# Optimization experiments

Measured on AMD Instinct MI355X. Metric: run time of the kernel, lower is better.

Reference implementation:

```python
import jax, jax.numpy as jnp
import numpy as np

GROUP_SIZE = 128
IN_FEATURES = 4096
OUT_FEATURES = 11008
BATCH = 16


def setup_inputs() -> dict:
    key = jax.random.key(0)
    k_x, k_q, k_s, k_z, k_b = jax.random.split(key, 5)
    num_groups = IN_FEATURES // GROUP_SIZE
    x = jax.random.normal(k_x, (BATCH, IN_FEATURES), dtype=jnp.float32)
    # packed int4 pairs stored as bytes in [0, 256)
    qweight = jax.random.randint(k_q, (OUT_FEATURES, IN_FEATURES // 2), 0, 256, dtype=jnp.int32)
    # positive scales of realistic magnitude, zeros in [0, 15]
    scales = jax.random.uniform(k_s, (OUT_FEATURES, num_groups), dtype=jnp.float32) * 0.01 + 1e-4
    zeros = jax.random.uniform(k_z, (OUT_FEATURES, num_groups), dtype=jnp.float32) * 15.0
    bias = jax.random.normal(k_b, (OUT_FEATURES,), dtype=jnp.float32)
    return {"x": x, "qweight": qweight, "scales": scales, "zeros": zeros, "bias": bias}


def _unpack_int4(packed, in_features):
    # packed: [O, I//2] ints in [0,256); low nibble is even column, high nibble odd
    low = packed & 15
    high = (packed >> 4) & 15
    return jnp.stack([low, high], axis=-1).reshape(packed.shape[0], in_features)  # [O, I]


def reference(x, qweight, scales, zeros, bias):
    q = _unpack_int4(qweight, IN_FEATURES).astype(jnp.float32)        # [O, I]
    s = jnp.repeat(scales, GROUP_SIZE, axis=1)                        # [O, I]
    z = jnp.repeat(zeros, GROUP_SIZE, axis=1)                         # [O, I]
    w = (q - z) * s                                                   # dequantized weight [O, I]
    return x @ w.T + bias                                             # [B, O]
```

## Files before the change

kernel.cpp:

```cpp
#include <hip/hip_runtime.h>
#include <hip/hip_fp16.h>

#define IN_F   4096
#define OUT_F  11008
#define BATCH  16
#define GROUPS 32
#define PPR    2048

typedef __attribute__((ext_vector_type(8))) _Float16 half8;
typedef __attribute__((ext_vector_type(2))) _Float16 h2;
typedef __attribute__((ext_vector_type(4))) float    float4_t;
typedef __attribute__((ext_vector_type(4))) int      int4_t;
typedef __attribute__((ext_vector_type(4))) unsigned uint4_t;

__device__ inline h2 cvt2(float a, float b) {
    return __builtin_bit_cast(h2, __builtin_amdgcn_cvt_pkrtz(a, b));
}

#define GLOAD_LDS(srcp, ldsp) \
    __builtin_amdgcn_global_load_lds( \
        (const __attribute__((address_space(1))) void*)(srcp), \
        (__attribute__((address_space(3))) void*)(ldsp), 16, 0, 0)

__global__ __launch_bounds__(256) void xcvt_perm(const float* __restrict__ x,
                                                 _Float16* __restrict__ xp) {
    const int T = blockIdx.x * 256 + threadIdx.x;
    const int step = T >> 6, lane = T & 63;
    const int b = lane & 15, k = step * 32 + (lane >> 4) * 8;
    const float4_t a0 = *(const float4_t*)(x + b * IN_F + k);
    const float4_t a1 = *(const float4_t*)(x + b * IN_F + k + 4);
    half8 h;
    h2 p0 = cvt2(a0.x, a0.y), p1 = cvt2(a0.z, a0.w);
    h2 p2 = cvt2(a1.x, a1.y), p3 = cvt2(a1.z, a1.w);
    h[0]=p0[0]; h[1]=p0[1]; h[2]=p1[0]; h[3]=p1[1];
    h[4]=p2[0]; h[5]=p2[1]; h[6]=p3[0]; h[7]=p3[1];
    *(half8*)(xp + step * 512 + lane * 8) = h;
}

__global__ __launch_bounds__(256) void gptq_gemm_w(
    const _Float16* __restrict__ xp, const int* __restrict__ qw,
    const float* __restrict__ scales, const float* __restrict__ zeros,
    float* __restrict__ ws_part)
{
    __shared__ int   lq[16 * 512];
    __shared__ float red[4][16][17];

    const int tid  = threadIdx.x;
    const int lane = tid & 63, wave = tid >> 6;
    const int otile = blockIdx.x >> 2, kq = blockIdx.x & 3;
    const int ln = lane & 15, lk = lane >> 4;
    const int o  = otile * 16 + ln;

    #pragma unroll
    for (int i = 0; i < 4; ++i) {
        const int row = wave * 4 + i;
        const int* src = qw + (otile * 16 + row) * PPR + kq * 512
                       + ((lane ^ (row & 7)) * 4);
        GLOAD_LDS(src, &lq[row * 512]);
    }

    const int c = wave;
    const int g = kq * 8 + c * 2;
    const float s0 = scales[o * GROUPS + g], s1 = scales[o * GROUPS + g + 1];
    const float z0 = zeros [o * GROUPS + g], z1 = zeros [o * GROUPS + g + 1];
    const h2 s2[2] = { cvt2(s0, s0), cvt2(s1, s1) };
    const h2 c2[2] = { cvt2(-z0 * s0, -z0 * s0), cvt2(-z1 * s1, -z1 * s1) };
    const h2 k1024 = { (_Float16)1024.0f, (_Float16)1024.0f };
    const int x3 = ln & 7;

    float4_t acc = {0.f, 0.f, 0.f, 0.f};

#define COMPUTE(C) { \
    _Pragma("unroll") \
    for (int t = 0; t < 8; ++t) { \
        const int4_t v = *(const int4_t*)((const char*)lq + ln * 2048 \
                        + (((C) * 32 + ((t * 4 + lk) ^ x3)) << 4)); \
        const half8 af = *(const half8*)(xp + (kq * 32 + (C) * 8 + t) * 512 \
                        + lane * 8); \
        const int gi = t >> 2; \
        uint4_t bw; \
        _Pragma("unroll") \
        for (int i = 0; i < 4; ++i) { \
            const unsigned pv = (unsigned)v[i]; \
            const unsigned u = (pv & 0xFu) | ((pv << 12) & 0xF0000u) \
                             | 0x64006400u;             \
            h2 q = __builtin_bit_cast(h2, u) - k1024;   \
            h2 w = q * s2[gi] + c2[gi];                 \
            bw[i] = __builtin_bit_cast(unsigned, w); \
        } \
        acc = __builtin_amdgcn_mfma_f32_16x16x32_f16( \
            af, __builtin_bit_cast(half8, bw), acc, 0, 0, 0); \
    } }

    __syncthreads();

    #pragma unroll
    for (int i = 0; i < 4; ++i) {
        const int row = wave * 4 + i;
        const int* src = qw + (otile * 16 + row) * PPR + kq * 512 + 256
                       + ((lane ^ (row & 7)) * 4);
        GLOAD_LDS(src, &lq[row * 512 + 256]);
    }

    if (wave < 2) COMPUTE(c)

    __syncthreads();

    if (wave >= 2) COMPUTE(c)

    #pragma unroll
    for (int r = 0; r < 4; ++r) red[wave][lk * 4 + r][ln] = acc[r];
    __syncthreads();

    const int row = tid >> 4, col = tid & 15;
    const float sum = red[0][row][col] + red[1][row][col]
                    + red[2][row][col] + red[3][row][col];
    ws_part[(kq * BATCH + row) * OUT_F + otile * 16 + col] = sum;
#undef COMPUTE
}

__global__ __launch_bounds__(256) void gptq_reduce(
    const float* __restrict__ ws_part, const float* __restrict__ bias,
    float* __restrict__ out)
{
    const int idx = blockIdx.x * 256 + threadIdx.x;
    if (idx >= BATCH * OUT_F) return;
    const int o = idx % OUT_F;
    out[idx] = bias[o]
             + ws_part[idx]
             + ws_part[1 * (BATCH * OUT_F) + idx]
             + ws_part[2 * (BATCH * OUT_F) + idx]
             + ws_part[3 * (BATCH * OUT_F) + idx];
}

__global__ __launch_bounds__(256) void gptq_gemm_fb(
    const float* __restrict__ x, const int* __restrict__ qw,
    const float* __restrict__ scales, const float* __restrict__ zeros,
    const float* __restrict__ bias, float* __restrict__ out)
{
    const int tid  = threadIdx.x;
    const int lane = tid & 63;
    const int wave = tid >> 6;
    const int otile = blockIdx.x;
    const int ln = lane & 15, lk = lane >> 4;
    const int o = otile * 16 + ln;
    const int kc0 = wave * 1024;

    const int* qbase = qw + o * PPR + (kc0 >> 1) + lk * 4;
    const float* srow = scales + o * GROUPS;
    const float* zrow = zeros  + o * GROUPS;

    float4_t acc = {0.f, 0.f, 0.f, 0.f};
    const h2 k1024 = { (_Float16)1024.0f, (_Float16)1024.0f };

    #pragma unroll
    for (int ch = 0; ch < 4; ++ch) {
        const int cc = kc0 + ch * 256;
        h2 s2[2], c2[2];
        #pragma unroll
        for (int gi = 0; gi < 2; ++gi) {
            const float s  = srow[(cc >> 7) + gi];
            const float c0 = -zrow[(cc >> 7) + gi] * s;
            s2[gi] = cvt2(s, s); c2[gi] = cvt2(c0, c0);
        }
        #pragma unroll
        for (int t = 0; t < 8; ++t) {
            const int4_t v = *(const int4_t*)(qbase + ch * 128 + t * 16);
            const float* xq = x + ln * IN_F + cc + t * 32 + lk * 8;
            const float4_t a0 = *(const float4_t*)(xq);
            const float4_t a1 = *(const float4_t*)(xq + 4);
            half8 af;
            h2 p0 = cvt2(a0.x, a0.y), p1 = cvt2(a0.z, a0.w);
            h2 p2 = cvt2(a1.x, a1.y), p3 = cvt2(a1.z, a1.w);
            af[0]=p0[0]; af[1]=p0[1]; af[2]=p1[0]; af[3]=p1[1];
            af[4]=p2[0]; af[5]=p2[1]; af[6]=p3[0]; af[7]=p3[1];
            const int gi = t >> 2;
            uint4_t bw;
            #pragma unroll
            for (int i = 0; i < 4; ++i) {
                const unsigned pv = (unsigned)v[i];
                const unsigned u = (pv & 0xFu) | ((pv << 12) & 0xF0000u)
                                 | 0x64006400u;
                h2 q = __builtin_bit_cast(h2, u) - k1024;
                h2 w = q * s2[gi] + c2[gi];
                bw[i] = __builtin_bit_cast(unsigned, w);
            }
            acc = __builtin_amdgcn_mfma_f32_16x16x32_f16(
                af, __builtin_bit_cast(half8, bw), acc, 0, 0, 0);
        }
    }

    __shared__ float red[4][16][17];
    #pragma unroll
    for (int r = 0; r < 4; ++r) red[wave][lk * 4 + r][ln] = acc[r];
    __syncthreads();
    const int row = tid >> 4, col = tid & 15;
    const float sum = red[0][row][col] + red[1][row][col]
                    + red[2][row][col] + red[3][row][col];
    const int oo = otile * 16 + col;
    out[row * OUT_F + oo] = sum + bias[oo];
}

extern "C" void kernel_launch(void* const* d_in, const int* in_sizes, int n_in,
                              void* d_out, int out_size, void* d_ws, size_t ws_size,
                              hipStream_t stream) {
    const float* x      = (const float*)d_in[0];
    const int*   qwgt   = (const int*)d_in[1];
    const float* scales = (const float*)d_in[2];
    const float* zeros  = (const float*)d_in[3];
    const float* bias   = (const float*)d_in[4];
    float* out = (float*)d_out;

    const int nOTiles = OUT_F / 16;
    const size_t need = (size_t)8 << 20;

    if (d_ws && ws_size >= need) {
        float*    ws_part = (float*)d_ws;
        _Float16* xp      = (_Float16*)((char*)d_ws + (4 << 20));
        hipLaunchKernelGGL(xcvt_perm, dim3(32), dim3(256), 0, stream, x, xp);
        hipLaunchKernelGGL(gptq_gemm_w, dim3(nOTiles * 4), dim3(256), 0, stream,
                           xp, qwgt, scales, zeros, ws_part);
        hipLaunchKernelGGL(gptq_reduce, dim3((BATCH * OUT_F + 255) / 256),
                           dim3(256), 0, stream, ws_part, bias, out);
    } else {
        hipLaunchKernelGGL(gptq_gemm_fb, dim3(nOTiles), dim3(256), 0, stream,
                           x, qwgt, scales, zeros, bias, out);
    }
}
```

Baseline: 30.61 us.

## Reschedule int4 GEMM loads with explicit waitcnts and vectorize reduce kernel

The main GEMM kernel now has each wave handle two groups (wave and wave+4) instead of two adjacent groups, so both halves of the LDS weight tile are consumed by all waves. It issues both async LDS weight loads up front and prefetches activations into registers with inline asm, using manual s_waitcnt vmcnt and s_barrier to overlap the second half's load with the first half's compute. The reduce kernel now works on float4 vectors. This relies on hand-counted vmcnt values, which are fragile if the compiler inserts other memory ops, and the pinned registers raise VGPR use.

```diff
diff --git a/kernel.cpp b/kernel.cpp
--- a/kernel.cpp
+++ b/kernel.cpp
@@ -50,63 +50,86 @@
     const int otile = blockIdx.x >> 2, kq = blockIdx.x & 3;
     const int ln = lane & 15, lk = lane >> 4;
     const int o  = otile * 16 + ln;
-
+    const int x3 = ln & 7;
+
+    const int gA = kq * 8 + wave, gB = gA + 4;
+    const float sa = scales[o * GROUPS + gA], za = zeros[o * GROUPS + gA];
+    const float sb = scales[o * GROUPS + gB], zb = zeros[o * GROUPS + gB];
+    const h2 s2a = cvt2(sa, sa), c2a = cvt2(-za * sa, -za * sa);
+    const h2 s2b = cvt2(sb, sb), c2b = cvt2(-zb * sb, -zb * sb);
+    const h2 k1024 = { (_Float16)1024.0f, (_Float16)1024.0f };
+
+    asm volatile("s_waitcnt vmcnt(0)" ::: "memory");
+    __builtin_amdgcn_sched_barrier(0);
+
+    const _Float16* xqa = xp + (kq * 32 + wave * 4) * 512 + lane * 8;
+    const _Float16* xqb = xqa + 16 * 512;
+    half8 xa0, xa1, xa2, xa3, xb0, xb1, xb2, xb3;
+    asm volatile("global_load_dwordx4 %0, %1, off"             : "=v"(xa0) : "v"(xqa));
+    asm volatile("global_load_dwordx4 %0, %1, off offset:1024" : "=v"(xa1) : "v"(xqa));
+    asm volatile("global_load_dwordx4 %0, %1, off offset:2048" : "=v"(xa2) : "v"(xqa));
+    asm volatile("global_load_dwordx4 %0, %1, off offset:3072" : "=v"(xa3) : "v"(xqa));
+    __builtin_amdgcn_sched_barrier(0);
     #pragma unroll
     for (int i = 0; i < 4; ++i) {
         const int row = wave * 4 + i;
-        const int* src = qw + (otile * 16 + row) * PPR + kq * 512
-                       + ((lane ^ (row & 7)) * 4);
-        GLOAD_LDS(src, &lq[row * 512]);
-    }
-
-    const int c = wave;
-    const int g = kq * 8 + c * 2;
-    const float s0 = scales[o * GROUPS + g], s1 = scales[o * GROUPS + g + 1];
-    const float z0 = zeros [o * GROUPS + g], z1 = zeros [o * GROUPS + g + 1];
-    const h2 s2[2] = { cvt2(s0, s0), cvt2(s1, s1) };
-    const h2 c2[2] = { cvt2(-z0 * s0, -z0 * s0), cvt2(-z1 * s1, -z1 * s1) };
-    const h2 k1024 = { (_Float16)1024.0f, (_Float16)1024.0f };
-    const int x3 = ln & 7;
-
-    float4_t acc = {0.f, 0.f, 0.f, 0.f};
-
-#define COMPUTE(C) { \
-    _Pragma("unroll") \
-    for (int t = 0; t < 8; ++t) { \
-        const int4_t v = *(const int4_t*)((const char*)lq + ln * 2048 \
-                        + (((C) * 32 + ((t * 4 + lk) ^ x3)) << 4)); \
-        const half8 af = *(const half8*)(xp + (kq * 32 + (C) * 8 + t) * 512 \
-                        + lane * 8); \
-        const int gi = t >> 2; \
-        uint4_t bw; \
-        _Pragma("unroll") \
-        for (int i = 0; i < 4; ++i) { \
-            const unsigned pv = (unsigned)v[i]; \
-            const unsigned u = (pv & 0xFu) | ((pv << 12) & 0xF0000u) \
-                             | 0x64006400u;             \
-            h2 q = __builtin_bit_cast(h2, u) - k1024;   \
-            h2 w = q * s2[gi] + c2[gi];                 \
-            bw[i] = __builtin_bit_cast(unsigned, w); \
-        } \
-        acc = __builtin_amdgcn_mfma_f32_16x16x32_f16( \
-            af, __builtin_bit_cast(half8, bw), acc, 0, 0, 0); \
-    } }
-
-    __syncthreads();
-
+        const int* s0 = qw + (otile * 16 + row) * PPR + kq * 512
+                      + ((lane ^ (row & 7)) * 4);
+        GLOAD_LDS(s0, &lq[row * 512]);
+    }
     #pragma unroll
     for (int i = 0; i < 4; ++i) {
         const int row = wave * 4 + i;
-        const int* src = qw + (otile * 16 + row) * PPR + kq * 512 + 256
-                       + ((lane ^ (row & 7)) * 4);
-        GLOAD_LDS(src, &lq[row * 512 + 256]);
-    }
-
-    if (wave < 2) COMPUTE(c)
-
-    __syncthreads();
-
-    if (wave >= 2) COMPUTE(c)
+        const int* s1 = qw + (otile * 16 + row) * PPR + kq * 512 + 256
+                      + ((lane ^ (row & 7)) * 4);
+        GLOAD_LDS(s1, &lq[row * 512 + 256]);
+    }
+    __builtin_amdgcn_sched_barrier(0);
+    asm volatile("s_waitcnt vmcnt(4)" ::: "memory");
+    __builtin_amdgcn_sched_barrier(0);
+    __builtin_amdgcn_s_barrier();
+    __builtin_amdgcn_sched_barrier(0);
+
+    asm volatile("global_load_dwordx4 %0, %1, off"             : "=v"(xb0) : "v"(xqb));
+    asm volatile("global_load_dwordx4 %0, %1, off offset:1024" : "=v"(xb1) : "v"(xqb));
+    asm volatile("global_load_dwordx4 %0, %1, off offset:2048" : "=v"(xb2) : "v"(xqb));
+    asm volatile("global_load_dwordx4 %0, %1, off offset:3072" : "=v"(xb3) : "v"(xqb));
+    __builtin_amdgcn_sched_barrier(0);
+
+    float4_t acc = {0.f, 0.f, 0.f, 0.f};
+
+#define STEP(XF, BB, T, S2, C2) { \
+    const int4_t v = *(const int4_t*)((const char*)lq + ln * 2048 + (BB) \
+                    + ((wave * 16 + (((T) * 4 + lk) ^ x3)) << 4)); \
+    uint4_t bw; \
+    _Pragma("unroll") \
+    for (int i = 0; i < 4; ++i) { \
+        const unsigned pv = (unsigned)v[i]; \
+        const unsigned u = (pv & 0xFu) | ((pv << 12) & 0xF0000u) \
+                         | 0x64006400u;             \
+        h2 q = __builtin_bit_cast(h2, u) - k1024;   \
+        h2 w = q * (S2) + (C2);                     \
+        bw[i] = __builtin_bit_cast(unsigned, w); \
+    } \
+    acc = __builtin_amdgcn_mfma_f32_16x16x32_f16( \
+        (XF), __builtin_bit_cast(half8, bw), acc, 0, 0, 0); }
+
+    STEP(xa0, 0, 0, s2a, c2a)
+    STEP(xa1, 0, 1, s2a, c2a)
+    STEP(xa2, 0, 2, s2a, c2a)
+    STEP(xa3, 0, 3, s2a, c2a)
+
+    __builtin_amdgcn_sched_barrier(0);
+    asm volatile("s_waitcnt vmcnt(0)" ::: "memory");
+    __builtin_amdgcn_sched_barrier(0);
+    __builtin_amdgcn_s_barrier();
+    __builtin_amdgcn_sched_barrier(0);
+
+    STEP(xb0, 1024, 0, s2b, c2b)
+    STEP(xb1, 1024, 1, s2b, c2b)
+    STEP(xb2, 1024, 2, s2b, c2b)
+    STEP(xb3, 1024, 3, s2b, c2b)
+#undef STEP
 
     #pragma unroll
     for (int r = 0; r < 4; ++r) red[wave][lk * 4 + r][ln] = acc[r];
@@ -116,21 +139,22 @@
     const float sum = red[0][row][col] + red[1][row][col]
                     + red[2][row][col] + red[3][row][col];
     ws_part[(kq * BATCH + row) * OUT_F + otile * 16 + col] = sum;
-#undef COMPUTE
 }
 
 __global__ __launch_bounds__(256) void gptq_reduce(
     const float* __restrict__ ws_part, const float* __restrict__ bias,
     float* __restrict__ out)
 {
-    const int idx = blockIdx.x * 256 + threadIdx.x;
-    if (idx >= BATCH * OUT_F) return;
-    const int o = idx % OUT_F;
-    out[idx] = bias[o]
-             + ws_part[idx]
-             + ws_part[1 * (BATCH * OUT_F) + idx]
-             + ws_part[2 * (BATCH * OUT_F) + idx]
-             + ws_part[3 * (BATCH * OUT_F) + idx];
+    const int i4 = (blockIdx.x * 256 + threadIdx.x) * 4;
+    if (i4 >= BATCH * OUT_F) return;
+    const int N = BATCH * OUT_F;
+    const int o = i4 % OUT_F;
+    const float4_t b  = *(const float4_t*)(bias + o);
+    const float4_t a0 = *(const float4_t*)(ws_part + i4);
+    const float4_t a1 = *(const float4_t*)(ws_part + N + i4);
+    const float4_t a2 = *(const float4_t*)(ws_part + 2 * N + i4);
+    const float4_t a3 = *(const float4_t*)(ws_part + 3 * N + i4);
+    *(float4_t*)((float*)out + i4) = b + a0 + a1 + a2 + a3;
 }
 
 __global__ __launch_bounds__(256) void gptq_gemm_fb(
@@ -220,7 +244,7 @@
         hipLaunchKernelGGL(xcvt_perm, dim3(32), dim3(256), 0, stream, x, xp);
         hipLaunchKernelGGL(gptq_gemm_w, dim3(nOTiles * 4), dim3(256), 0, stream,
                            xp, qwgt, scales, zeros, ws_part);
-        hipLaunchKernelGGL(gptq_reduce, dim3((BATCH * OUT_F + 255) / 256),
+        hipLaunchKernelGGL(gptq_reduce, dim3((BATCH * OUT_F / 4 + 255) / 256),
                            dim3(256), 0, stream, ws_part, bias, out);
     } else {
         hipLaunchKernelGGL(gptq_gemm_fb, dim3(nOTiles), dim3(256), 0, stream,
```

After: 30.31 us. Within noise of the previous version (-1.0%).

## Fuse split-K GEMM and reduce into one full-K kernel with double-buffered LDS

Applied to the files above, without the earlier changes.

Replaces the four-way split-K GEMM plus separate reduction kernel with a single kernel per 16-output tile. It walks all four K chunks with double-buffered LDS weight staging, register-prefetched activations, and manual vmcnt waits. The bias add is fused into the final store. This removes the partial-sum workspace traffic and one launch, but cuts the grid to 688 blocks, which lowers parallelism on a large GPU and relies on hand-written wait counts being correct.

```diff
diff --git a/kernel.cpp b/kernel.cpp
--- a/kernel.cpp
+++ b/kernel.cpp
@@ -37,47 +37,79 @@
     *(half8*)(xp + step * 512 + lane * 8) = h;
 }
 
-__global__ __launch_bounds__(256) void gptq_gemm_w(
+__global__ __launch_bounds__(256) void gptq_gemm_full(
     const _Float16* __restrict__ xp, const int* __restrict__ qw,
     const float* __restrict__ scales, const float* __restrict__ zeros,
-    float* __restrict__ ws_part)
+    const float* __restrict__ bias, float* __restrict__ out)
 {
-    __shared__ int   lq[16 * 512];
+    __shared__ int   lq[2][16 * 512];
     __shared__ float red[4][16][17];
 
     const int tid  = threadIdx.x;
     const int lane = tid & 63, wave = tid >> 6;
-    const int otile = blockIdx.x >> 2, kq = blockIdx.x & 3;
+    const int otile = blockIdx.x;
     const int ln = lane & 15, lk = lane >> 4;
     const int o  = otile * 16 + ln;
-
-    #pragma unroll
-    for (int i = 0; i < 4; ++i) {
-        const int row = wave * 4 + i;
-        const int* src = qw + (otile * 16 + row) * PPR + kq * 512
-                       + ((lane ^ (row & 7)) * 4);
-        GLOAD_LDS(src, &lq[row * 512]);
+    const int x3 = ln & 7;
+
+    h2 s2g[8], c2g[8];
+    #pragma unroll
+    for (int c = 0; c < 4; ++c) {
+        #pragma unroll
+        for (int gi = 0; gi < 2; ++gi) {
+            const int g = c * 8 + wave * 2 + gi;
+            const float s = scales[o * GROUPS + g];
+            const float z = zeros [o * GROUPS + g];
+            s2g[c * 2 + gi] = cvt2(s, s);
+            c2g[c * 2 + gi] = cvt2(-z * s, -z * s);
+        }
     }
-
-    const int c = wave;
-    const int g = kq * 8 + c * 2;
-    const float s0 = scales[o * GROUPS + g], s1 = scales[o * GROUPS + g + 1];
-    const float z0 = zeros [o * GROUPS + g], z1 = zeros [o * GROUPS + g + 1];
-    const h2 s2[2] = { cvt2(s0, s0), cvt2(s1, s1) };
-    const h2 c2[2] = { cvt2(-z0 * s0, -z0 * s0), cvt2(-z1 * s1, -z1 * s1) };
     const h2 k1024 = { (_Float16)1024.0f, (_Float16)1024.0f };
-    const int x3 = ln & 7;
-
+
+    asm volatile("s_waitcnt vmcnt(0)" ::: "memory");
+    __builtin_amdgcn_sched_barrier(0);
+
+    half8 xv[2][8];
     float4_t acc = {0.f, 0.f, 0.f, 0.f};
 
-#define COMPUTE(C) { \
+#define STAGE(C, BUF) { \
+    _Pragma("unroll") \
+    for (int i = 0; i < 4; ++i) { \
+        const int row = wave * 4 + i; \
+        const int* s0 = qw + (otile * 16 + row) * PPR + (C) * 512 \
+                      + ((lane ^ (row & 7)) * 4); \
+        GLOAD_LDS(s0, &lq[BUF][row * 512]); \
+        GLOAD_LDS(s0 + 256, &lq[BUF][row * 512 + 256]); \
+    } \
+    __builtin_amdgcn_sched_barrier(0); }
+
+#define XLOAD(C, BUF) { \
+    const char* xc = (const char*)xp + ((C) * 32 + wave * 8) * 1024 + lane * 16; \
+    asm volatile("global_load_dwordx4 %0, %1, off"             : "=v"(xv[BUF][0]) : "v"(xc)); \
+    asm volatile("global_load_dwordx4 %0, %1, off offset:1024" : "=v"(xv[BUF][1]) : "v"(xc)); \
+    asm volatile("global_load_dwordx4 %0, %1, off offset:2048" : "=v"(xv[BUF][2]) : "v"(xc)); \
+    asm volatile("global_load_dwordx4 %0, %1, off offset:3072" : "=v"(xv[BUF][3]) : "v"(xc)); \
+    const char* xd = xc + 4096; \
+    asm volatile("global_load_dwordx4 %0, %1, off"             : "=v"(xv[BUF][4]) : "v"(xd)); \
+    asm volatile("global_load_dwordx4 %0, %1, off offset:1024" : "=v"(xv[BUF][5]) : "v"(xd)); \
+    asm volatile("global_load_dwordx4 %0, %1, off offset:2048" : "=v"(xv[BUF][6]) : "v"(xd)); \
+    asm volatile("global_load_dwordx4 %0, %1, off offset:3072" : "=v"(xv[BUF][7]) : "v"(xd)); \
+    __builtin_amdgcn_sched_barrier(0); }
+
+#define WAITV16 { asm volatile("s_waitcnt vmcnt(16)" ::: "memory"); \
+                  __builtin_amdgcn_sched_barrier(0); }
+#define WAITV0  { asm volatile("s_waitcnt vmcnt(0)"  ::: "memory"); \
+                  __builtin_amdgcn_sched_barrier(0); }
+#define BARR    { __builtin_amdgcn_s_barrier(); \
+                  __builtin_amdgcn_sched_barrier(0); }
+
+#define COMPUTE(C, BUF) { \
     _Pragma("unroll") \
     for (int t = 0; t < 8; ++t) { \
-        const int4_t v = *(const int4_t*)((const char*)lq + ln * 2048 \
-                        + (((C) * 32 + ((t * 4 + lk) ^ x3)) << 4)); \
-        const half8 af = *(const half8*)(xp + (kq * 32 + (C) * 8 + t) * 512 \
-                        + lane * 8); \
-        const int gi = t >> 2; \
+        const int4_t v = *(const int4_t*)((const char*)lq \
+            + (BUF) * 32768 + ln * 2048 + (wave >> 1) * 1024 \
+            + ((((wave & 1) * 32 + t * 4 + lk) ^ x3) << 4)); \
+        const int sg = (C) * 2 + (t >> 2); \
         uint4_t bw; \
         _Pragma("unroll") \
         for (int i = 0; i < 4; ++i) { \
@@ -85,28 +117,34 @@
             const unsigned u = (pv & 0xFu) | ((pv << 12) & 0xF0000u) \
                              | 0x64006400u;             \
             h2 q = __builtin_bit_cast(h2, u) - k1024;   \
-            h2 w = q * s2[gi] + c2[gi];                 \
+            h2 w = q * s2g[sg] + c2g[sg];               \
             bw[i] = __builtin_bit_cast(unsigned, w); \
         } \
         acc = __builtin_amdgcn_mfma_f32_16x16x32_f16( \
-            af, __builtin_bit_cast(half8, bw), acc, 0, 0, 0); \
+            xv[BUF][t], __builtin_bit_cast(half8, bw), acc, 0, 0, 0); \
     } }
 
-    __syncthreads();
-
-    #pragma unroll
-    for (int i = 0; i < 4; ++i) {
-        const int row = wave * 4 + i;
-        const int* src = qw + (otile * 16 + row) * PPR + kq * 512 + 256
-                       + ((lane ^ (row & 7)) * 4);
-        GLOAD_LDS(src, &lq[row * 512 + 256]);
-    }
-
-    if (wave < 2) COMPUTE(c)
-
-    __syncthreads();
-
-    if (wave >= 2) COMPUTE(c)
+    STAGE(0, 0) XLOAD(0, 0)
+    STAGE(1, 1) XLOAD(1, 1)
+    WAITV16 BARR
+    COMPUTE(0, 0)
+    BARR
+    STAGE(2, 0) XLOAD(2, 0)
+    WAITV16 BARR
+    COMPUTE(1, 1)
+    BARR
+    STAGE(3, 1) XLOAD(3, 1)
+    WAITV16 BARR
+    COMPUTE(2, 0)
+    WAITV0 BARR
+    COMPUTE(3, 1)
+
+#undef STAGE
+#undef XLOAD
+#undef WAITV16
+#undef WAITV0
+#undef BARR
+#undef COMPUTE
 
     #pragma unroll
     for (int r = 0; r < 4; ++r) red[wave][lk * 4 + r][ln] = acc[r];
@@ -115,22 +153,8 @@
     const int row = tid >> 4, col = tid & 15;
     const float sum = red[0][row][col] + red[1][row][col]
                     + red[2][row][col] + red[3][row][col];
-    ws_part[(kq * BATCH + row) * OUT_F + otile * 16 + col] = sum;
-#undef COMPUTE
-}
-
-__global__ __launch_bounds__(256) void gptq_reduce(
-    const float* __restrict__ ws_part, const float* __restrict__ bias,
-    float* __restrict__ out)
-{
-    const int idx = blockIdx.x * 256 + threadIdx.x;
-    if (idx >= BATCH * OUT_F) return;
-    const int o = idx % OUT_F;
-    out[idx] = bias[o]
-             + ws_part[idx]
-             + ws_part[1 * (BATCH * OUT_F) + idx]
-             + ws_part[2 * (BATCH * OUT_F) + idx]
-             + ws_part[3 * (BATCH * OUT_F) + idx];
+    const int oo = otile * 16 + col;
+    out[row * OUT_F + oo] = sum + bias[oo];
 }
 
 __global__ __launch_bounds__(256) void gptq_gemm_fb(
@@ -212,16 +236,12 @@
     float* out = (float*)d_out;
 
     const int nOTiles = OUT_F / 16;
-    const size_t need = (size_t)8 << 20;
-
-    if (d_ws && ws_size >= need) {
-        float*    ws_part = (float*)d_ws;
-        _Float16* xp      = (_Float16*)((char*)d_ws + (4 << 20));
+
+    if (d_ws && ws_size >= (size_t)(1 << 20)) {
+        _Float16* xp = (_Float16*)d_ws;
         hipLaunchKernelGGL(xcvt_perm, dim3(32), dim3(256), 0, stream, x, xp);
-        hipLaunchKernelGGL(gptq_gemm_w, dim3(nOTiles * 4), dim3(256), 0, stream,
-                           xp, qwgt, scales, zeros, ws_part);
-        hipLaunchKernelGGL(gptq_reduce, dim3((BATCH * OUT_F + 255) / 256),
-                           dim3(256), 0, stream, ws_part, bias, out);
+        hipLaunchKernelGGL(gptq_gemm_full, dim3(nOTiles), dim3(256), 0, stream,
+                           xp, qwgt, scales, zeros, bias, out);
     } else {
         hipLaunchKernelGGL(gptq_gemm_fb, dim3(nOTiles), dim3(256), 0, stream,
                            x, qwgt, scales, zeros, bias, out);
```

Result: faster. 29.83 us, median of 2 (-2.6%).

## Replace LDS-staged split-K GEMM with single-wave register double-buffered split-8 kernel

Applied to the files above, without the earlier changes.

Replaces the 256-thread block that staged packed weights through LDS with 64-thread single-wave blocks. Each block loads weights and activations straight into registers with inline-asm global loads, double-buffered by explicit vmcnt waits. Split-K grows from 4 to 8, which gives more in-flight blocks and memory parallelism for the bandwidth-bound int32 weight stream and removes barriers and the LDS reduction. The trade-off is twice as much partial-sum traffic. The reduce kernel is vectorized to sum 8 partials with float4 loads.

```diff
diff --git a/kernel.cpp b/kernel.cpp
--- a/kernel.cpp
+++ b/kernel.cpp
@@ -16,11 +16,6 @@
 __device__ inline h2 cvt2(float a, float b) {
     return __builtin_bit_cast(h2, __builtin_amdgcn_cvt_pkrtz(a, b));
 }
-
-#define GLOAD_LDS(srcp, ldsp) \
-    __builtin_amdgcn_global_load_lds( \
-        (const __attribute__((address_space(1))) void*)(srcp), \
-        (__attribute__((address_space(3))) void*)(ldsp), 16, 0, 0)
 
 __global__ __launch_bounds__(256) void xcvt_perm(const float* __restrict__ x,
                                                  _Float16* __restrict__ xp) {
@@ -37,100 +32,108 @@
     *(half8*)(xp + step * 512 + lane * 8) = h;
 }
 
-__global__ __launch_bounds__(256) void gptq_gemm_w(
+__global__ __launch_bounds__(64, 5) void gptq_gemm_s8(
     const _Float16* __restrict__ xp, const int* __restrict__ qw,
     const float* __restrict__ scales, const float* __restrict__ zeros,
     float* __restrict__ ws_part)
 {
-    __shared__ int   lq[16 * 512];
-    __shared__ float red[4][16][17];
-
-    const int tid  = threadIdx.x;
-    const int lane = tid & 63, wave = tid >> 6;
-    const int otile = blockIdx.x >> 2, kq = blockIdx.x & 3;
-    const int ln = lane & 15, lk = lane >> 4;
+    const int lane  = threadIdx.x;
+    const int otile = blockIdx.x >> 3;
+    const int kq    = blockIdx.x & 7;
+
+    const int ln = lane & 15;
+    const int lk = lane >> 4;
     const int o  = otile * 16 + ln;
 
-    #pragma unroll
-    for (int i = 0; i < 4; ++i) {
-        const int row = wave * 4 + i;
-        const int* src = qw + (otile * 16 + row) * PPR + kq * 512
-                       + ((lane ^ (row & 7)) * 4);
-        GLOAD_LDS(src, &lq[row * 512]);
+    const float4_t sf = *(const float4_t*)(scales + o * GROUPS + kq * 4);
+    const float4_t zf = *(const float4_t*)(zeros  + o * GROUPS + kq * 4);
+    h2 s2g[4], c2g[4];
+    {
+        const float sa[4] = { sf.x, sf.y, sf.z, sf.w };
+        const float za[4] = { zf.x, zf.y, zf.z, zf.w };
+        #pragma unroll
+        for (int c = 0; c < 4; ++c) {
+            s2g[c] = cvt2(sa[c], sa[c]);
+            c2g[c] = cvt2(-za[c] * sa[c], -za[c] * sa[c]);
+        }
     }
-
-    const int c = wave;
-    const int g = kq * 8 + c * 2;
-    const float s0 = scales[o * GROUPS + g], s1 = scales[o * GROUPS + g + 1];
-    const float z0 = zeros [o * GROUPS + g], z1 = zeros [o * GROUPS + g + 1];
-    const h2 s2[2] = { cvt2(s0, s0), cvt2(s1, s1) };
-    const h2 c2[2] = { cvt2(-z0 * s0, -z0 * s0), cvt2(-z1 * s1, -z1 * s1) };
     const h2 k1024 = { (_Float16)1024.0f, (_Float16)1024.0f };
-    const int x3 = ln & 7;
-
+
+    asm volatile("s_waitcnt vmcnt(0)" ::: "memory");
+    __builtin_amdgcn_sched_barrier(0);
+
+    const char* qb = (const char*)(qw + o * PPR + kq * 256 + lk * 4);
+    const char* xb = (const char*)xp + (kq * 16) * 1024 + lane * 16;
+
+    int4_t qv[2][4];
+    half8  xv[2][4];
     float4_t acc = {0.f, 0.f, 0.f, 0.f};
 
-#define COMPUTE(C) { \
+#define LOADSUB(C, B) { \
+    const char* qc = qb + (C) * 256; \
+    const char* xc = xb + (C) * 4096; \
+    asm volatile("global_load_dwordx4 %0, %1, off"            : "=v"(qv[B][0]) : "v"(qc)); \
+    asm volatile("global_load_dwordx4 %0, %1, off offset:64"  : "=v"(qv[B][1]) : "v"(qc)); \
+    asm volatile("global_load_dwordx4 %0, %1, off offset:128" : "=v"(qv[B][2]) : "v"(qc)); \
+    asm volatile("global_load_dwordx4 %0, %1, off offset:192" : "=v"(qv[B][3]) : "v"(qc)); \
+    asm volatile("global_load_dwordx4 %0, %1, off"             : "=v"(xv[B][0]) : "v"(xc)); \
+    asm volatile("global_load_dwordx4 %0, %1, off offset:1024" : "=v"(xv[B][1]) : "v"(xc)); \
+    asm volatile("global_load_dwordx4 %0, %1, off offset:2048" : "=v"(xv[B][2]) : "v"(xc)); \
+    asm volatile("global_load_dwordx4 %0, %1, off offset:3072" : "=v"(xv[B][3]) : "v"(xc)); \
+    __builtin_amdgcn_sched_barrier(0); }
+
+#define WAITV8 { asm volatile("s_waitcnt vmcnt(8)" ::: "memory"); \
+                 __builtin_amdgcn_sched_barrier(0); }
+#define WAITV0 { asm volatile("s_waitcnt vmcnt(0)" ::: "memory"); \
+                 __builtin_amdgcn_sched_barrier(0); }
+
+#define COMPUTE(C, B) { \
     _Pragma("unroll") \
-    for (int t = 0; t < 8; ++t) { \
-        const int4_t v = *(const int4_t*)((const char*)lq + ln * 2048 \
-                        + (((C) * 32 + ((t * 4 + lk) ^ x3)) << 4)); \
-        const half8 af = *(const half8*)(xp + (kq * 32 + (C) * 8 + t) * 512 \
-                        + lane * 8); \
-        const int gi = t >> 2; \
+    for (int t = 0; t < 4; ++t) { \
         uint4_t bw; \
         _Pragma("unroll") \
         for (int i = 0; i < 4; ++i) { \
-            const unsigned pv = (unsigned)v[i]; \
+            const unsigned pv = (unsigned)qv[B][t][i]; \
             const unsigned u = (pv & 0xFu) | ((pv << 12) & 0xF0000u) \
                              | 0x64006400u;             \
             h2 q = __builtin_bit_cast(h2, u) - k1024;   \
-            h2 w = q * s2[gi] + c2[gi];                 \
+            h2 w = q * s2g[C] + c2g[C];                 \
             bw[i] = __builtin_bit_cast(unsigned, w); \
         } \
         acc = __builtin_amdgcn_mfma_f32_16x16x32_f16( \
-            af, __builtin_bit_cast(half8, bw), acc, 0, 0, 0); \
+            xv[B][t], __builtin_bit_cast(half8, bw), acc, 0, 0, 0); \
     } }
 
-    __syncthreads();
-
-    #pragma unroll
-    for (int i = 0; i < 4; ++i) {
-        const int row = wave * 4 + i;
-        const int* src = qw + (otile * 16 + row) * PPR + kq * 512 + 256
-                       + ((lane ^ (row & 7)) * 4);
-        GLOAD_LDS(src, &lq[row * 512 + 256]);
-    }
-
-    if (wave < 2) COMPUTE(c)
-
-    __syncthreads();
-
-    if (wave >= 2) COMPUTE(c)
-
-    #pragma unroll
-    for (int r = 0; r < 4; ++r) red[wave][lk * 4 + r][ln] = acc[r];
-    __syncthreads();
-
-    const int row = tid >> 4, col = tid & 15;
-    const float sum = red[0][row][col] + red[1][row][col]
-                    + red[2][row][col] + red[3][row][col];
-    ws_part[(kq * BATCH + row) * OUT_F + otile * 16 + col] = sum;
+    LOADSUB(0, 0)
+    LOADSUB(1, 1)
+    WAITV8  COMPUTE(0, 0) LOADSUB(2, 0)
+    WAITV8  COMPUTE(1, 1) LOADSUB(3, 1)
+    WAITV8  COMPUTE(2, 0)
+    WAITV0  COMPUTE(3, 1)
+
+#undef LOADSUB
+#undef WAITV8
+#undef WAITV0
 #undef COMPUTE
-}
-
-__global__ __launch_bounds__(256) void gptq_reduce(
+
+    #pragma unroll
+    for (int r = 0; r < 4; ++r)
+        ws_part[(kq * BATCH + lk * 4 + r) * OUT_F + otile * 16 + ln] = acc[r];
+}
+
+__global__ __launch_bounds__(256) void gptq_reduce8(
     const float* __restrict__ ws_part, const float* __restrict__ bias,
     float* __restrict__ out)
 {
-    const int idx = blockIdx.x * 256 + threadIdx.x;
-    if (idx >= BATCH * OUT_F) return;
-    const int o = idx % OUT_F;
-    out[idx] = bias[o]
-             + ws_part[idx]
-             + ws_part[1 * (BATCH * OUT_F) + idx]
-             + ws_part[2 * (BATCH * OUT_F) + idx]
-             + ws_part[3 * (BATCH * OUT_F) + idx];
+    const int i4 = (blockIdx.x * 256 + threadIdx.x) * 4;
+    if (i4 >= BATCH * OUT_F) return;
+    const int N = BATCH * OUT_F;
+    const int o = i4 % OUT_F;
+    float4_t s = *(const float4_t*)(bias + o);
+    #pragma unroll
+    for (int k = 0; k < 8; ++k)
+        s += *(const float4_t*)(ws_part + k * N + i4);
+    *(float4_t*)((float*)out + i4) = s;
 }
 
 __global__ __launch_bounds__(256) void gptq_gemm_fb(
@@ -216,11 +219,11 @@
 
     if (d_ws && ws_size >= need) {
         float*    ws_part = (float*)d_ws;
-        _Float16* xp      = (_Float16*)((char*)d_ws + (4 << 20));
+        _Float16* xp      = (_Float16*)((char*)d_ws + (6 << 20));
         hipLaunchKernelGGL(xcvt_perm, dim3(32), dim3(256), 0, stream, x, xp);
-        hipLaunchKernelGGL(gptq_gemm_w, dim3(nOTiles * 4), dim3(256), 0, stream,
+        hipLaunchKernelGGL(gptq_gemm_s8, dim3(nOTiles * 8), dim3(64), 0, stream,
                            xp, qwgt, scales, zeros, ws_part);
-        hipLaunchKernelGGL(gptq_reduce, dim3((BATCH * OUT_F + 255) / 256),
+        hipLaunchKernelGGL(gptq_reduce8, dim3(BATCH * OUT_F / 4 / 256),
                            dim3(256), 0, stream, ws_part, bias, out);
     } else {
         hipLaunchKernelGGL(gptq_gemm_fb, dim3(nOTiles), dim3(256), 0, stream,
```

New measurement: 31.01 us. About the same (+1.3%).
